# Kernel tuning notes

Hardware: AMD Instinct MI355X
Metric: run time of the kernel (lower is better)

Reference implementation:

```python
import jax, jax.numpy as jnp
import numpy as np

D_MODEL = 1024
N_HEADS = 16
D_K = D_MODEL // N_HEADS


def setup_inputs() -> dict:
    key = jax.random.key(0)
    ks = jax.random.split(key, 9)
    B, S = 4, 2048
    scale = 1.0 / np.sqrt(D_MODEL)
    x = jax.random.normal(ks[0], (B, S, D_MODEL), dtype=jnp.float32)
    # Linear params: weight [out,in] (torch convention), bias [out]
    wq = jax.random.uniform(ks[1], (D_MODEL, D_MODEL), jnp.float32, -scale, scale)
    bq = jax.random.uniform(ks[2], (D_MODEL,), jnp.float32, -scale, scale)
    wk = jax.random.uniform(ks[3], (D_MODEL, D_MODEL), jnp.float32, -scale, scale)
    bk = jax.random.uniform(ks[4], (D_MODEL,), jnp.float32, -scale, scale)
    wv = jax.random.uniform(ks[5], (D_MODEL, D_MODEL), jnp.float32, -scale, scale)
    bv = jax.random.uniform(ks[6], (D_MODEL,), jnp.float32, -scale, scale)
    wo = jax.random.uniform(ks[7], (D_MODEL, D_MODEL), jnp.float32, -scale, scale)
    bo = jax.random.uniform(ks[8], (D_MODEL,), jnp.float32, -scale, scale)
    return {"x": x, "wq": wq, "bq": bq, "wk": wk, "bk": bk,
            "wv": wv, "bv": bv, "wo": wo, "bo": bo}


def reference(x, wq, bq, wk, bk, wv, bv, wo, bo):
    B, S, _ = x.shape
    # QKV projections (torch Linear: x @ W^T + b)
    q = x @ wq.T + bq
    k = x @ wk.T + bk
    v = x @ wv.T + bv
    # [B, H, S, D_K]
    q = q.reshape(B, S, N_HEADS, D_K).transpose(0, 2, 1, 3)
    k = k.reshape(B, S, N_HEADS, D_K).transpose(0, 2, 1, 3)
    v = v.reshape(B, S, N_HEADS, D_K).transpose(0, 2, 1, 3)
    scores = jnp.einsum('bhqd,bhkd->bhqk', q, k) / jnp.sqrt(jnp.float32(D_K))
    attn = jax.nn.softmax(scores, axis=-1)
    out = jnp.einsum('bhqk,bhkd->bhqd', attn, v)
    out = out.transpose(0, 2, 1, 3).reshape(B, S, D_MODEL)
    return out @ wo.T + bo
```

## Files before the change

kernel.cpp:

```cpp
#include <hip/hip_runtime.h>

#define DMODEL 1024
#define NHEADS 16
#define DK 64
#define BATCH 4
#define SEQ 2048
#define MROWS (BATCH * SEQ)
#define NT 16

typedef __attribute__((ext_vector_type(8))) short bf16x8;
typedef __attribute__((ext_vector_type(8))) unsigned short u16x8;
typedef __attribute__((ext_vector_type(4))) unsigned short u16x4;
typedef __attribute__((ext_vector_type(4))) float f32x4;
typedef __attribute__((ext_vector_type(16))) float f32x16;
typedef __attribute__((ext_vector_type(2))) unsigned int u32x2;
typedef __attribute__((ext_vector_type(4))) unsigned int u32x4;

using gld_gptr = const __attribute__((address_space(1))) unsigned int*;
using gld_lptr = __attribute__((address_space(3))) unsigned int*;

#define QSCALE 0.18033688011112042f

__device__ inline unsigned short f32_bf16(float f) {
    unsigned int u = __float_as_uint(f);
    u += 0x7FFFu + ((u >> 16) & 1u);
    return (unsigned short)(u >> 16);
}

__device__ inline unsigned int cvtpk_bf16(float a, float b) {
    unsigned int r;
    asm("v_cvt_pk_bf16_f32 %0, %1, %2" : "=v"(r) : "v"(a), "v"(b));
    return r;
}

__device__ inline f32x16 fz16() {
    f32x16 v;
#pragma unroll
    for (int i = 0; i < 16; ++i) v[i] = 0.f;
    return v;
}

struct Conv5 {
    const float* s[5];
    unsigned short* d[5];
};

__global__ __launch_bounds__(256) void conv5_kernel(Conv5 c) {
    int bx = blockIdx.x;
    int which, idx;
    if (bx < 4096) { which = 0; idx = bx; }
    else { which = 1 + ((bx - 4096) >> 9); idx = (bx - 4096) & 511; }
    int i = idx * 256 + threadIdx.x;
    const float4* s = (const float4*)(c.s[which] + (size_t)i * 8);
    float4 a = s[0], b = s[1];
    u16x8 o;
    o[0] = f32_bf16(a.x); o[1] = f32_bf16(a.y); o[2] = f32_bf16(a.z); o[3] = f32_bf16(a.w);
    o[4] = f32_bf16(b.x); o[5] = f32_bf16(b.y); o[6] = f32_bf16(b.z); o[7] = f32_bf16(b.w);
    *(u16x8*)(c.d[which] + (size_t)i * 8) = o;
}

__device__ __forceinline__ void stage_half(const unsigned short* mat, int row0, int step,
                                           char* lds_half, int tid) {
#pragma unroll
    for (int rnd = 0; rnd < 2; ++rnd) {
        int rl = rnd * 64 + (tid >> 3);
        int c16 = (tid & 7) ^ (rl & 7);
        const unsigned short* g = mat + (size_t)(row0 + rl) * DMODEL + step * 64 + c16 * 8;
        __builtin_amdgcn_global_load_lds((gld_gptr)g,
            (gld_lptr)(lds_half + rnd * 8192 + (tid >> 6) * 1024), 16, 0, 0);
    }
}

__device__ __forceinline__ bf16x8 lds_frag(const char* base, int row, int kk, int l) {
    int kb = kk * 64 + (l >> 4) * 16;
    return *(const bf16x8*)(base + row * 128 + (kb ^ ((row & 7) << 4)));
}

template <int QP>
__device__ __forceinline__ void phase_reads(const char* Ab, const char* Bb,
                                            bf16x8 (&breg)[4][2], bf16x8 (&areg)[2],
                                            int wm, int wn, int l) {
    int l15 = l & 15;
    if constexpr (QP == 0) {
#pragma unroll
        for (int nt = 0; nt < 4; ++nt)
#pragma unroll
            for (int kk = 0; kk < 2; ++kk)
                breg[nt][kk] = lds_frag(Bb, wn * 64 + nt * 16 + l15, kk, l);
    }
#pragma unroll
    for (int kk = 0; kk < 2; ++kk)
        areg[kk] = lds_frag(Ab, wm * 64 + QP * 16 + l15, kk, l);
}

template <int QP>
__device__ __forceinline__ void phase_mfma(bf16x8 (&areg)[2], bf16x8 (&breg)[4][2],
                                           f32x4 (&acc)[4][4]) {
    __builtin_amdgcn_s_setprio(1);
#pragma unroll
    for (int nt = 0; nt < 4; ++nt) {
        acc[QP][nt] = __builtin_amdgcn_mfma_f32_16x16x32_bf16(
            areg[0], breg[nt][0], acc[QP][nt], 0, 0, 0);
        acc[QP][nt] = __builtin_amdgcn_mfma_f32_16x16x32_bf16(
            areg[1], breg[nt][1], acc[QP][nt], 0, 0, 0);
    }
    __builtin_amdgcn_s_setprio(0);
}

#define GBAR() __builtin_amdgcn_s_barrier()
#define VMC2() asm volatile("s_waitcnt vmcnt(2)" ::: "memory")

template <bool F32OUT>
__device__ __forceinline__ void gemm_core(const unsigned short* __restrict__ Am,
                                          const unsigned short* __restrict__ Bm,
                                          const float* __restrict__ bias, void* Cv,
                                          float scl, int m0, int n0) {
    __shared__ __align__(16) char lds[98304];
    char* A0 = lds;
    char* B0 = lds + 32768;
    char* A1 = lds + 49152;
    char* B1 = lds + 81920;

    int tid = threadIdx.x, l = tid & 63, w = tid >> 6;
    int wm = w >> 1, wn = w & 1;

    f32x4 acc[4][4];
#pragma unroll
    for (int i = 0; i < 4; ++i)
#pragma unroll
        for (int j = 0; j < 4; ++j) acc[i][j] = (f32x4){0.f, 0.f, 0.f, 0.f};

    stage_half(Am, m0,       0, A0,         tid);
    stage_half(Am, m0 + 128, 0, A0 + 16384, tid);
    stage_half(Bm, n0,       0, B0,         tid);
    stage_half(Bm, n0,       1, B1,         tid);
    VMC2();
    GBAR();

    bf16x8 breg[4][2];
    for (int i = 0; i < NT / 2; ++i) {
        int E = 2 * i;
        bf16x8 areg[2];
        phase_reads<0>(A0, B0, breg, areg, wm, wn, l);
        stage_half(Am, m0,       (E + 1) & 15, A1, tid);
        GBAR(); phase_mfma<0>(areg, breg, acc); GBAR();

        phase_reads<1>(A0, B0, breg, areg, wm, wn, l);
        stage_half(Am, m0 + 128, (E + 1) & 15, A1 + 16384, tid);
        GBAR(); phase_mfma<1>(areg, breg, acc); GBAR();

        phase_reads<2>(A0, B0, breg, areg, wm, wn, l);
        stage_half(Bm, n0,       (E + 2) & 15, B0, tid);
        GBAR(); phase_mfma<2>(areg, breg, acc); GBAR();

        phase_reads<3>(A0, B0, breg, areg, wm, wn, l);
        GBAR(); phase_mfma<3>(areg, breg, acc);
        VMC2();
        GBAR();

        phase_reads<0>(A1, B1, breg, areg, wm, wn, l);
        stage_half(Am, m0,       (E + 2) & 15, A0, tid);
        GBAR(); phase_mfma<0>(areg, breg, acc); GBAR();

        phase_reads<1>(A1, B1, breg, areg, wm, wn, l);
        stage_half(Am, m0 + 128, (E + 2) & 15, A0 + 16384, tid);
        GBAR(); phase_mfma<1>(areg, breg, acc); GBAR();

        phase_reads<2>(A1, B1, breg, areg, wm, wn, l);
        stage_half(Bm, n0,       (E + 3) & 15, B1, tid);
        GBAR(); phase_mfma<2>(areg, breg, acc); GBAR();

        phase_reads<3>(A1, B1, breg, areg, wm, wn, l);
        GBAR(); phase_mfma<3>(areg, breg, acc);
        VMC2();
        GBAR();
    }

    int lm = l >> 4, ln = l & 15;
#pragma unroll
    for (int nt = 0; nt < 4; ++nt) {
        int col = n0 + wn * 64 + nt * 16 + ln;
        float bv = bias[col];
#pragma unroll
        for (int mt = 0; mt < 4; ++mt)
#pragma unroll
            for (int r = 0; r < 4; ++r) {
                int row = m0 + wm * 64 + mt * 16 + lm * 4 + r;
                float v = (acc[mt][nt][r] + bv) * scl;
                if constexpr (F32OUT)
                    ((float*)Cv)[(size_t)row * DMODEL + col] = v;
                else
                    ((unsigned short*)Cv)[(size_t)row * DMODEL + col] = f32_bf16(v);
            }
    }
}

struct QkvPtrs {
    const unsigned short* w[3];
    const float* b[3];
    unsigned short* c[3];
    float scale[3];
};

__global__ __launch_bounds__(512, 2) void gemm_qkv8(const unsigned short* __restrict__ A, QkvPtrs p) {
    int sel = blockIdx.y >> 3;
    int n0 = (blockIdx.y & 7) * 128;
    int m0 = blockIdx.x * 256;
    gemm_core<false>(A, p.w[sel], p.b[sel], p.c[sel], p.scale[sel], m0, n0);
}

__global__ __launch_bounds__(512, 2) void gemm_out8(const unsigned short* __restrict__ A,
                                                    const unsigned short* __restrict__ B,
                                                    const float* __restrict__ bias,
                                                    float* __restrict__ C) {
    gemm_core<true>(A, B, bias, C, 1.0f, blockIdx.x * 256, blockIdx.y * 128);
}

#define BUILD_PW(dst, pv, o)                                                        \
    {                                                                               \
        unsigned int wa_ = cvtpk_bf16(pv[(o) + 0], pv[(o) + 1]);                    \
        unsigned int wb_ = cvtpk_bf16(pv[(o) + 2], pv[(o) + 3]);                    \
        unsigned int wc_ = cvtpk_bf16(pv[(o) + 4], pv[(o) + 5]);                    \
        unsigned int wd_ = cvtpk_bf16(pv[(o) + 6], pv[(o) + 7]);                    \
        u32x2 ra_ = __builtin_amdgcn_permlane32_swap(wa_, wc_, false, false);       \
        u32x2 rb_ = __builtin_amdgcn_permlane32_swap(wb_, wd_, false, false);       \
        dst = (u32x4){ra_[0], rb_[0], ra_[1], rb_[1]};                              \
    }

#define ABAR() asm volatile("s_barrier" ::: "memory")
#define AVMC0() asm volatile("s_waitcnt vmcnt(0)" ::: "memory")

__device__ __forceinline__ void stage_k(const unsigned short* kp, int kt,
                                        unsigned short* kbuf, int l, int w) {
#pragma unroll
    for (int i = 0; i < 2; ++i) {
        int chunk = w + i * 4;
        int srccol = (l & 7) ^ (l >> 3);
        const unsigned short* g = kp + (size_t)(kt * 64 + chunk * 8 + (l >> 3)) * DMODEL + srccol * 8;
        __builtin_amdgcn_global_load_lds((gld_gptr)g, (gld_lptr)(kbuf + chunk * 512), 16, 0, 0);
    }
}

__device__ __forceinline__ void load_v(const unsigned short* vp, int kt, int tid,
                                       bf16x8& va, bf16x8& vb) {
    int kvp = (tid & 31) * 2;
    int d0 = (tid >> 5) * 8;
    va = *(const bf16x8*)&vp[(size_t)(kt * 64 + kvp) * DMODEL + d0];
    vb = *(const bf16x8*)&vp[(size_t)(kt * 64 + kvp + 1) * DMODEL + d0];
}

__device__ __forceinline__ void write_v(unsigned short* vbuf, int tid, bf16x8 va, bf16x8 vb) {
    int kvp = (tid & 31) * 2;
    int d0 = (tid >> 5) * 8;
#pragma unroll
    for (int j = 0; j < 8; ++j) {
        int d = d0 + j;
        unsigned int val = ((unsigned int)(unsigned short)va[j]) |
                           (((unsigned int)(unsigned short)vb[j]) << 16);
        int byt = d * 128 + (((kvp >> 3) ^ (d & 7)) << 4) + (kvp & 7) * 2;
        *(unsigned int*)((char*)vbuf + byt) = val;
    }
}

__global__ __launch_bounds__(256, 2) void attn_kernel(const unsigned short* __restrict__ Q,
                                                      const unsigned short* __restrict__ Km,
                                                      const unsigned short* __restrict__ Vm,
                                                      unsigned short* __restrict__ O) {
    __shared__ unsigned short Klds[2][64 * 64];
    __shared__ unsigned short Vt[2][64 * 64];

    int flat = blockIdx.y * gridDim.x + blockIdx.x;
    int xcd = flat & 7, idx = flat >> 3;
    int bh = xcd * 8 + (idx & 7);
    int qt = idx >> 3;
    int b = bh >> 4, h = bh & 15;
    int tid = threadIdx.x, l = tid & 63, w = tid >> 6;
    int lq = l & 31, hf = l >> 5;
    const size_t base = ((size_t)b * SEQ) * DMODEL + (size_t)h * DK;
    const unsigned short* qp = Q + base;
    const unsigned short* kp = Km + base;
    const unsigned short* vp = Vm + base;
    int q0 = qt * 256 + w * 64;

    bf16x8 qf[2][4];
#pragma unroll
    for (int sb = 0; sb < 2; ++sb)
#pragma unroll
        for (int ks = 0; ks < 4; ++ks)
            qf[sb][ks] = *(const bf16x8*)&qp[(size_t)(q0 + sb * 32 + lq) * DMODEL + ks * 16 + hf * 8];

    f32x16 accO[2][2];
    accO[0][0] = fz16(); accO[0][1] = fz16(); accO[1][0] = fz16(); accO[1][1] = fz16();
    float l_r[2] = {0.f, 0.f};

    bf16x8 va, vb;
    stage_k(kp, 0, Klds[0], l, w);
    load_v(vp, 0, tid, va, vb);
    AVMC0();
    write_v(Vt[0], tid, va, vb);
    ABAR();

    for (int kt = 0; kt < SEQ / 64; ++kt) {
        int cur = kt & 1, nxt = cur ^ 1;
        bool pre = (kt + 1 < SEQ / 64);
        if (pre) {
            stage_k(kp, kt + 1, Klds[nxt], l, w);
            load_v(vp, kt + 1, tid, va, vb);
        }

        f32x16 s[2][2];
        s[0][0] = fz16(); s[0][1] = fz16(); s[1][0] = fz16(); s[1][1] = fz16();
#pragma unroll
        for (int ks = 0; ks < 4; ++ks) {
            int col16 = ks * 2 + hf;
            bf16x8 kf0 = *(const bf16x8*)((const char*)Klds[cur] + lq * 128 + ((col16 ^ (lq & 7)) << 4));
            bf16x8 kf1 = *(const bf16x8*)((const char*)Klds[cur] + (lq + 32) * 128 + ((col16 ^ (lq & 7)) << 4));
            s[0][0] = __builtin_amdgcn_mfma_f32_32x32x16_bf16(kf0, qf[0][ks], s[0][0], 0, 0, 0);
            s[0][1] = __builtin_amdgcn_mfma_f32_32x32x16_bf16(kf1, qf[0][ks], s[0][1], 0, 0, 0);
            s[1][0] = __builtin_amdgcn_mfma_f32_32x32x16_bf16(kf0, qf[1][ks], s[1][0], 0, 0, 0);
            s[1][1] = __builtin_amdgcn_mfma_f32_32x32x16_bf16(kf1, qf[1][ks], s[1][1], 0, 0, 0);
        }

        float rs0 = 0.f;
#pragma unroll
        for (int r = 0; r < 16; ++r) { s[0][0][r] = __builtin_amdgcn_exp2f(s[0][0][r]); rs0 += s[0][0][r]; }
#pragma unroll
        for (int r = 0; r < 16; ++r) { s[0][1][r] = __builtin_amdgcn_exp2f(s[0][1][r]); rs0 += s[0][1][r]; }
        rs0 += __shfl_xor(rs0, 32);
        l_r[0] += rs0;
        u32x4 pw0[4];
        BUILD_PW(pw0[0], s[0][0], 0);
        BUILD_PW(pw0[1], s[0][0], 8);
        BUILD_PW(pw0[2], s[0][1], 0);
        BUILD_PW(pw0[3], s[0][1], 8);

        float rs1 = 0.f;
#pragma unroll
        for (int ks = 0; ks < 4; ++ks) {
            int o = (ks & 1) * 8;
            u32x4 pw1;
            if (ks < 2) {
#pragma unroll
                for (int r = 0; r < 8; ++r) { s[1][0][o + r] = __builtin_amdgcn_exp2f(s[1][0][o + r]); rs1 += s[1][0][o + r]; }
                BUILD_PW(pw1, s[1][0], o);
            } else {
#pragma unroll
                for (int r = 0; r < 8; ++r) { s[1][1][o + r] = __builtin_amdgcn_exp2f(s[1][1][o + r]); rs1 += s[1][1][o + r]; }
                BUILD_PW(pw1, s[1][1], o);
            }
            int col16 = ks * 2 + hf;
            int d1 = 32 + lq;
            bf16x8 vf0 = *(const bf16x8*)((const char*)Vt[cur] + lq * 128 + ((col16 ^ (lq & 7)) << 4));
            bf16x8 vf1 = *(const bf16x8*)((const char*)Vt[cur] + d1 * 128 + ((col16 ^ (d1 & 7)) << 4));
            bf16x8 pf0 = *(bf16x8*)&pw0[ks];
            bf16x8 pf1 = *(bf16x8*)&pw1;
            accO[0][0] = __builtin_amdgcn_mfma_f32_32x32x16_bf16(vf0, pf0, accO[0][0], 0, 0, 0);
            accO[0][1] = __builtin_amdgcn_mfma_f32_32x32x16_bf16(vf1, pf0, accO[0][1], 0, 0, 0);
            accO[1][0] = __builtin_amdgcn_mfma_f32_32x32x16_bf16(vf0, pf1, accO[1][0], 0, 0, 0);
            accO[1][1] = __builtin_amdgcn_mfma_f32_32x32x16_bf16(vf1, pf1, accO[1][1], 0, 0, 0);
        }
        rs1 += __shfl_xor(rs1, 32);
        l_r[1] += rs1;

        if (pre) {
            AVMC0();
            write_v(Vt[nxt], tid, va, vb);
        }
        ABAR();
    }

#pragma unroll
    for (int sb = 0; sb < 2; ++sb) {
        float inv = 1.0f / l_r[sb];
        unsigned short* op = O + base + (size_t)(q0 + sb * 32 + lq) * DMODEL;
#pragma unroll
        for (int db = 0; db < 2; ++db)
#pragma unroll
            for (int rg = 0; rg < 4; ++rg) {
                int dbase = db * 32 + rg * 8 + hf * 4;
                u16x4 ov;
#pragma unroll
                for (int j = 0; j < 4; ++j) ov[j] = f32_bf16(accO[sb][db][rg * 4 + j] * inv);
                *(u16x4*)&op[dbase] = ov;
            }
    }
}

extern "C" void kernel_launch(void* const* d_in, const int* in_sizes, int n_in,
                              void* d_out, int out_size, void* d_ws, size_t ws_size,
                              hipStream_t stream) {
    (void)in_sizes; (void)n_in; (void)out_size; (void)ws_size;
    const float* x  = (const float*)d_in[0];
    const float* wq = (const float*)d_in[1];
    const float* bq = (const float*)d_in[2];
    const float* wk = (const float*)d_in[3];
    const float* bk = (const float*)d_in[4];
    const float* wv = (const float*)d_in[5];
    const float* bv = (const float*)d_in[6];
    const float* wo = (const float*)d_in[7];
    const float* bo = (const float*)d_in[8];
    float* out = (float*)d_out;
    char* ws = (char*)d_ws;

    unsigned short* xb  = (unsigned short*)(ws);
    unsigned short* wqb = (unsigned short*)(ws + (16ull << 20));
    unsigned short* wkb = (unsigned short*)(ws + (18ull << 20));
    unsigned short* wvb = (unsigned short*)(ws + (20ull << 20));
    unsigned short* wob = (unsigned short*)(ws + (22ull << 20));
    unsigned short* qb  = (unsigned short*)(ws + (24ull << 20));
    unsigned short* kb  = (unsigned short*)(ws + (40ull << 20));
    unsigned short* vb  = (unsigned short*)(ws + (56ull << 20));
    unsigned short* ob  = xb;

    Conv5 cv;
    cv.s[0] = x;  cv.d[0] = xb;
    cv.s[1] = wq; cv.d[1] = wqb;
    cv.s[2] = wk; cv.d[2] = wkb;
    cv.s[3] = wv; cv.d[3] = wvb;
    cv.s[4] = wo; cv.d[4] = wob;
    conv5_kernel<<<4096 + 4 * 512, 256, 0, stream>>>(cv);

    QkvPtrs p;
    p.w[0] = wqb; p.w[1] = wkb; p.w[2] = wvb;
    p.b[0] = bq;  p.b[1] = bk;  p.b[2] = bv;
    p.c[0] = qb;  p.c[1] = kb;  p.c[2] = vb;
    p.scale[0] = QSCALE; p.scale[1] = 1.0f; p.scale[2] = 1.0f;
    gemm_qkv8<<<dim3(32, 24), 512, 0, stream>>>(xb, p);

    attn_kernel<<<dim3(8, 64), 256, 0, stream>>>(qb, kb, vb, ob);

    gemm_out8<<<dim3(32, 8), 512, 0, stream>>>(ob, wob, bo, out);
}
```

Measured before the change: 171.6 us.

## Fuse x fp32-to-bf16 conversion into QKV GEMM A-tile staging

Drops x from the standalone conversion kernel. The QKV GEMM now loads fp32 x tiles into registers, converts them to bf16 with v_cvt_pk_bf16, and writes them into the swizzled LDS layout itself. This removes a 32MB read plus 16MB write-and-reread pass through the workspace. In exchange the GEMM reads A as fp32 (twice the bytes, and repeated across 24 N-blocks), uses extra registers, and replaces async global_load_lds with register staging and added waits.

```diff
diff --git a/kernel.cpp b/kernel.cpp
--- a/kernel.cpp
+++ b/kernel.cpp
@@ -40,16 +40,14 @@
     return v;
 }
 
-struct Conv5 {
-    const float* s[5];
-    unsigned short* d[5];
+struct Conv4 {
+    const float* s[4];
+    unsigned short* d[4];
 };
 
-__global__ __launch_bounds__(256) void conv5_kernel(Conv5 c) {
+__global__ __launch_bounds__(256) void conv4_kernel(Conv4 c) {
     int bx = blockIdx.x;
-    int which, idx;
-    if (bx < 4096) { which = 0; idx = bx; }
-    else { which = 1 + ((bx - 4096) >> 9); idx = (bx - 4096) & 511; }
+    int which = bx >> 9, idx = bx & 511;
     int i = idx * 256 + threadIdx.x;
     const float4* s = (const float4*)(c.s[which] + (size_t)i * 8);
     float4 a = s[0], b = s[1];
@@ -71,6 +69,30 @@
     }
 }
 
+__device__ __forceinline__ void loadA_half(const float* x, int row0, int step, int tid,
+                                           float4 (&r)[4]) {
+#pragma unroll
+    for (int rnd = 0; rnd < 2; ++rnd) {
+        int rl = rnd * 64 + (tid >> 3);
+        int c16 = (tid & 7) ^ (rl & 7);
+        const float* g = x + (size_t)(row0 + rl) * DMODEL + step * 64 + c16 * 8;
+        r[rnd * 2 + 0] = *(const float4*)(g);
+        r[rnd * 2 + 1] = *(const float4*)(g + 4);
+    }
+}
+
+__device__ __forceinline__ void writeA_half(char* lds_half, int tid, float4 (&r)[4]) {
+#pragma unroll
+    for (int rnd = 0; rnd < 2; ++rnd) {
+        u32x4 wv;
+        wv[0] = cvtpk_bf16(r[rnd * 2 + 0].x, r[rnd * 2 + 0].y);
+        wv[1] = cvtpk_bf16(r[rnd * 2 + 0].z, r[rnd * 2 + 0].w);
+        wv[2] = cvtpk_bf16(r[rnd * 2 + 1].x, r[rnd * 2 + 1].y);
+        wv[3] = cvtpk_bf16(r[rnd * 2 + 1].z, r[rnd * 2 + 1].w);
+        *(u32x4*)(lds_half + rnd * 8192 + (tid >> 6) * 1024 + (tid & 63) * 16) = wv;
+    }
+}
+
 __device__ __forceinline__ bf16x8 lds_frag(const char* base, int row, int kk, int l) {
     int kb = kk * 64 + (l >> 4) * 16;
     return *(const bf16x8*)(base + row * 128 + (kb ^ ((row & 7) << 4)));
@@ -109,9 +131,11 @@
 
 #define GBAR() __builtin_amdgcn_s_barrier()
 #define VMC2() asm volatile("s_waitcnt vmcnt(2)" ::: "memory")
-
-template <bool F32OUT>
-__device__ __forceinline__ void gemm_core(const unsigned short* __restrict__ Am,
+#define VMC4() asm volatile("s_waitcnt vmcnt(4)" ::: "memory")
+#define LGKM0() asm volatile("s_waitcnt lgkmcnt(0)" ::: "memory")
+
+template <bool F32OUT, bool F32A>
+__device__ __forceinline__ void gemm_core(const void* __restrict__ Amv,
                                           const unsigned short* __restrict__ Bm,
                                           const float* __restrict__ bias, void* Cv,
                                           float scl, int m0, int n0) {
@@ -124,55 +148,87 @@
     int tid = threadIdx.x, l = tid & 63, w = tid >> 6;
     int wm = w >> 1, wn = w & 1;
 
+    const unsigned short* Am16 = (const unsigned short*)Amv;
+    const float* Am32 = (const float*)Amv;
+
     f32x4 acc[4][4];
 #pragma unroll
     for (int i = 0; i < 4; ++i)
 #pragma unroll
         for (int j = 0; j < 4; ++j) acc[i][j] = (f32x4){0.f, 0.f, 0.f, 0.f};
 
-    stage_half(Am, m0,       0, A0,         tid);
-    stage_half(Am, m0 + 128, 0, A0 + 16384, tid);
-    stage_half(Bm, n0,       0, B0,         tid);
-    stage_half(Bm, n0,       1, B1,         tid);
-    VMC2();
-    GBAR();
+    float4 rA0[4], rA1[4];
+
+    if constexpr (F32A) {
+        loadA_half(Am32, m0,       0, tid, rA0);
+        loadA_half(Am32, m0 + 128, 0, tid, rA1);
+        stage_half(Bm, n0, 0, B0, tid);
+        stage_half(Bm, n0, 1, B1, tid);
+        VMC4();
+        writeA_half(A0,         tid, rA0);
+        writeA_half(A0 + 16384, tid, rA1);
+        VMC2();
+        LGKM0();
+        GBAR();
+    } else {
+        stage_half(Am16, m0,       0, A0,         tid);
+        stage_half(Am16, m0 + 128, 0, A0 + 16384, tid);
+        stage_half(Bm, n0, 0, B0, tid);
+        stage_half(Bm, n0, 1, B1, tid);
+        VMC2();
+        GBAR();
+    }
 
     bf16x8 breg[4][2];
     for (int i = 0; i < NT / 2; ++i) {
         int E = 2 * i;
         bf16x8 areg[2];
         phase_reads<0>(A0, B0, breg, areg, wm, wn, l);
-        stage_half(Am, m0,       (E + 1) & 15, A1, tid);
+        if constexpr (F32A) loadA_half(Am32, m0,       (E + 1) & 15, tid, rA0);
+        else                stage_half(Am16, m0,       (E + 1) & 15, A1, tid);
         GBAR(); phase_mfma<0>(areg, breg, acc); GBAR();
 
         phase_reads<1>(A0, B0, breg, areg, wm, wn, l);
-        stage_half(Am, m0 + 128, (E + 1) & 15, A1 + 16384, tid);
+        if constexpr (F32A) loadA_half(Am32, m0 + 128, (E + 1) & 15, tid, rA1);
+        else                stage_half(Am16, m0 + 128, (E + 1) & 15, A1 + 16384, tid);
         GBAR(); phase_mfma<1>(areg, breg, acc); GBAR();
 
         phase_reads<2>(A0, B0, breg, areg, wm, wn, l);
-        stage_half(Bm, n0,       (E + 2) & 15, B0, tid);
+        stage_half(Bm, n0, (E + 2) & 15, B0, tid);
         GBAR(); phase_mfma<2>(areg, breg, acc); GBAR();
 
         phase_reads<3>(A0, B0, breg, areg, wm, wn, l);
         GBAR(); phase_mfma<3>(areg, breg, acc);
         VMC2();
+        if constexpr (F32A) {
+            writeA_half(A1,         tid, rA0);
+            writeA_half(A1 + 16384, tid, rA1);
+            LGKM0();
+        }
         GBAR();
 
         phase_reads<0>(A1, B1, breg, areg, wm, wn, l);
-        stage_half(Am, m0,       (E + 2) & 15, A0, tid);
+        if constexpr (F32A) loadA_half(Am32, m0,       (E + 2) & 15, tid, rA0);
+        else                stage_half(Am16, m0,       (E + 2) & 15, A0, tid);
         GBAR(); phase_mfma<0>(areg, breg, acc); GBAR();
 
         phase_reads<1>(A1, B1, breg, areg, wm, wn, l);
-        stage_half(Am, m0 + 128, (E + 2) & 15, A0 + 16384, tid);
+        if constexpr (F32A) loadA_half(Am32, m0 + 128, (E + 2) & 15, tid, rA1);
+        else                stage_half(Am16, m0 + 128, (E + 2) & 15, A0 + 16384, tid);
         GBAR(); phase_mfma<1>(areg, breg, acc); GBAR();
 
         phase_reads<2>(A1, B1, breg, areg, wm, wn, l);
-        stage_half(Bm, n0,       (E + 3) & 15, B1, tid);
+        stage_half(Bm, n0, (E + 3) & 15, B1, tid);
         GBAR(); phase_mfma<2>(areg, breg, acc); GBAR();
 
         phase_reads<3>(A1, B1, breg, areg, wm, wn, l);
         GBAR(); phase_mfma<3>(areg, breg, acc);
         VMC2();
+        if constexpr (F32A) {
+            writeA_half(A0,         tid, rA0);
+            writeA_half(A0 + 16384, tid, rA1);
+            LGKM0();
+        }
         GBAR();
     }
 
@@ -202,18 +258,18 @@
     float scale[3];
 };
 
-__global__ __launch_bounds__(512, 2) void gemm_qkv8(const unsigned short* __restrict__ A, QkvPtrs p) {
+__global__ __launch_bounds__(512, 2) void gemm_qkv8(const float* __restrict__ X, QkvPtrs p) {
     int sel = blockIdx.y >> 3;
     int n0 = (blockIdx.y & 7) * 128;
     int m0 = blockIdx.x * 256;
-    gemm_core<false>(A, p.w[sel], p.b[sel], p.c[sel], p.scale[sel], m0, n0);
+    gemm_core<false, true>(X, p.w[sel], p.b[sel], p.c[sel], p.scale[sel], m0, n0);
 }
 
 __global__ __launch_bounds__(512, 2) void gemm_out8(const unsigned short* __restrict__ A,
                                                     const unsigned short* __restrict__ B,
                                                     const float* __restrict__ bias,
                                                     float* __restrict__ C) {
-    gemm_core<true>(A, B, bias, C, 1.0f, blockIdx.x * 256, blockIdx.y * 128);
+    gemm_core<true, false>(A, B, bias, C, 1.0f, blockIdx.x * 256, blockIdx.y * 128);
 }
 
 #define BUILD_PW(dst, pv, o)                                                        \
@@ -402,7 +458,7 @@
     float* out = (float*)d_out;
     char* ws = (char*)d_ws;
 
-    unsigned short* xb  = (unsigned short*)(ws);
+    unsigned short* ob  = (unsigned short*)(ws);
     unsigned short* wqb = (unsigned short*)(ws + (16ull << 20));
     unsigned short* wkb = (unsigned short*)(ws + (18ull << 20));
     unsigned short* wvb = (unsigned short*)(ws + (20ull << 20));
@@ -410,22 +466,20 @@
     unsigned short* qb  = (unsigned short*)(ws + (24ull << 20));
     unsigned short* kb  = (unsigned short*)(ws + (40ull << 20));
     unsigned short* vb  = (unsigned short*)(ws + (56ull << 20));
-    unsigned short* ob  = xb;
-
-    Conv5 cv;
-    cv.s[0] = x;  cv.d[0] = xb;
-    cv.s[1] = wq; cv.d[1] = wqb;
-    cv.s[2] = wk; cv.d[2] = wkb;
-    cv.s[3] = wv; cv.d[3] = wvb;
-    cv.s[4] = wo; cv.d[4] = wob;
-    conv5_kernel<<<4096 + 4 * 512, 256, 0, stream>>>(cv);
+
+    Conv4 cv;
+    cv.s[0] = wq; cv.d[0] = wqb;
+    cv.s[1] = wk; cv.d[1] = wkb;
+    cv.s[2] = wv; cv.d[2] = wvb;
+    cv.s[3] = wo; cv.d[3] = wob;
+    conv4_kernel<<<4 * 512, 256, 0, stream>>>(cv);
 
     QkvPtrs p;
     p.w[0] = wqb; p.w[1] = wkb; p.w[2] = wvb;
     p.b[0] = bq;  p.b[1] = bk;  p.b[2] = bv;
     p.c[0] = qb;  p.c[1] = kb;  p.c[2] = vb;
     p.scale[0] = QSCALE; p.scale[1] = 1.0f; p.scale[2] = 1.0f;
-    gemm_qkv8<<<dim3(32, 24), 512, 0, stream>>>(xb, p);
+    gemm_qkv8<<<dim3(32, 24), 512, 0, stream>>>(x, p);
 
     attn_kernel<<<dim3(8, 64), 256, 0, stream>>>(qb, kb, vb, ob);
 
```

New measurement: 184.7 us. 1.08x slower.
